# Performance work log

Measured on AMD Instinct MI355X. Metric: run time of the kernel, lower is better.

Reference implementation:

```python
import jax, jax.numpy as jnp
import numpy as np

N_NODES = 50000
N_EDGES = 400000
N_E2E = 1600000
F_N = 128
F_E = 64
H = 128
NEG_SLOPE = 0.2


def setup_inputs() -> dict:
    key = jax.random.key(0)
    ks = jax.random.split(key, 8)
    x_node = jax.random.normal(ks[0], (N_NODES, F_N), dtype=jnp.float32)
    edge_attr = jax.random.normal(ks[1], (N_EDGES, F_E), dtype=jnp.float32)
    edge_index = jax.random.randint(ks[2], (2, N_EDGES), 0, N_NODES, dtype=jnp.int64)
    edge_edge_index = jax.random.randint(ks[3], (2, N_E2E), 0, N_EDGES, dtype=jnp.int64)
    # xavier-uniform-like init scales
    def xavier(k, shape):
        fan_in, fan_out = shape[1], shape[0]
        lim = jnp.sqrt(6.0 / (fan_in + fan_out)).astype(jnp.float32)
        return jax.random.uniform(k, shape, jnp.float32, -lim, lim)
    Wn = xavier(ks[4], (H, F_N))          # lin_node.weight
    We = xavier(ks[5], (H, F_E))          # lin_edge.weight
    an = xavier(ks[6], (1, 2 * H))[0]     # att_n.weight, flattened to [2H]
    ae = xavier(ks[7], (1, 2 * H))[0]     # att_e.weight, flattened to [2H]
    return {"x_node": x_node, "edge_attr": edge_attr, "edge_index": edge_index,
            "edge_edge_index": edge_edge_index, "Wn": Wn, "We": We, "an": an, "ae": ae}


def _segment_softmax(score, seg, num_segments):
    m = jax.ops.segment_max(score, seg, num_segments=num_segments)
    ex = jnp.exp(score - m[seg])
    denom = jax.ops.segment_sum(ex, seg, num_segments=num_segments)
    return ex / denom[seg]


def reference(x_node, edge_attr, edge_index, edge_edge_index, Wn, We, an, ae):
    E = edge_attr.shape[0]
    h = x_node @ Wn.T      # [N, H]
    g = edge_attr @ We.T   # [E, H]

    # ---- node-based neighbors of each edge (its 2 endpoints) ----
    u, v = edge_index[0], edge_index[1]
    e_rep = jnp.concatenate([jnp.arange(E), jnp.arange(E)])   # segment ids [2E]
    n_for_e = jnp.concatenate([u, v])                          # [2E]
    a1, a2 = an[:H], an[H:]   # split cat([g, h]) @ an into two dots
    h_nbr = h[n_for_e]                                         # [2E, H]
    score_ne = jax.nn.leaky_relu(g[e_rep] @ a1 + h_nbr @ a2, NEG_SLOPE)
    alpha_ne = _segment_softmax(score_ne, e_rep, E)
    s_n = jax.ops.segment_sum(alpha_ne[:, None] * h_nbr, e_rep, num_segments=E)
    cnt_n = jax.ops.segment_sum(jnp.ones_like(alpha_ne), e_rep, num_segments=E)
    e_from_nodes = jax.nn.relu(s_n / jnp.maximum(cnt_n, 1.0)[:, None])

    # ---- edge-based neighbors (edges sharing a node) ----
    e_src, e_nbr = edge_edge_index[0], edge_edge_index[1]
    b1, b2 = ae[:H], ae[H:]
    g_nbr = g[e_nbr]                                           # [E2E, H]
    score_ee = jax.nn.leaky_relu(g[e_src] @ b1 + g_nbr @ b2, NEG_SLOPE)
    alpha_ee = _segment_softmax(score_ee, e_src, E)
    s_e = jax.ops.segment_sum(alpha_ee[:, None] * g_nbr, e_src, num_segments=E)
    cnt_e = jax.ops.segment_sum(jnp.ones_like(alpha_ee), e_src, num_segments=E)
    e_from_edges = jax.nn.relu(s_e / jnp.maximum(cnt_e, 1.0)[:, None])

    return jnp.concatenate([e_from_nodes, e_from_edges], axis=-1)  # [E, 2H]
```

## Files before the change

kernel.cpp:

```cpp
#include <hip/hip_runtime.h>
#include <hip/hip_bf16.h>

#define N_NODES 50000
#define N_EDGES 400000
#define N_E2E   1600000
#define F_N 128
#define F_E 64
#define H   128
#define NEG_SLOPE 0.2f
#define CAP 24

typedef __hip_bfloat16 bf16;
typedef __attribute__((ext_vector_type(8))) short bf16x8;
typedef __attribute__((ext_vector_type(4))) float f32x4;


__device__ inline float2 upk(unsigned int v) {
    union { unsigned int u; float f; } a, b;
    a.u = v << 16;
    b.u = v & 0xffff0000u;
    return make_float2(a.f, b.f);
}
__device__ inline unsigned int f2bfbits(float f) {
    union { float f; unsigned int u; } a; a.f = f;
    return (a.u + 0x7fffu + ((a.u >> 16) & 1u)) >> 16;
}
__device__ inline float lrelu(float x) { return x > 0.f ? x : NEG_SLOPE * x; }

__device__ inline float ldf(const void* p, size_t i, int isf32) {
    return isf32 ? ((const float*)p)[i] : __bfloat162float(((const bf16*)p)[i]);
}
__device__ inline int ldidx(const int* p, long long k, int is64) {
    return is64 ? p[2 * k] : p[k];
}

__device__ inline void loadA4(const void* p, int isf32, size_t idx, float* v) {
    if (isf32) {
        const float4 f = *(const float4*)((const float*)p + idx);
        v[0] = f.x; v[1] = f.y; v[2] = f.z; v[3] = f.w;
    } else {
        const uint2 u = *(const uint2*)((const bf16*)p + idx);
        float2 a = upk(u.x), b = upk(u.y);
        v[0] = a.x; v[1] = a.y; v[2] = b.x; v[3] = b.y;
    }
}
__device__ inline void stash(unsigned short* s, unsigned off, unsigned loOff, const float* v) {
    unsigned hb[4], lb[4];
    #pragma unroll
    for (int j = 0; j < 4; ++j) {
        unsigned hbits = f2bfbits(v[j]);
        union { unsigned u; float f; } hf; hf.u = hbits << 16;
        hb[j] = hbits;
        lb[j] = f2bfbits(v[j] - hf.f);
    }
    *(uint2*)((char*)s + off)         = make_uint2(hb[0] | (hb[1] << 16), hb[2] | (hb[3] << 16));
    *(uint2*)((char*)s + loOff + off) = make_uint2(lb[0] | (lb[1] << 16), lb[2] | (lb[3] << 16));
}

__global__ __launch_bounds__(256) void k_pat(unsigned int* __restrict__ o,
                                             long long n, unsigned int pat) {
    long long i = (long long)blockIdx.x * 256 + threadIdx.x;
    long long stride = (long long)gridDim.x * 256;
    for (; i < n; i += stride) o[i] = pat;
}

__global__ __launch_bounds__(256) void k_init(const unsigned int* x, const unsigned int* ea,
                                              const unsigned int* Wn, const unsigned int* We,
                                              const unsigned int* an, const unsigned int* ae,
                                              const unsigned int* ei, const unsigned int* eei,
                                              int* __restrict__ flags, int* __restrict__ cnt) {
    int i = blockIdx.x * 256 + threadIdx.x;
    if (i < N_EDGES) cnt[i] = 0;
    if (blockIdx.x == 0) {
        int t = threadIdx.x;
        if (t < 6) {
            const unsigned int* p = t == 0 ? x : t == 1 ? ea : t == 2 ? Wn
                                  : t == 3 ? We : t == 4 ? an : ae;
            int inrange = 0;
            for (int k = 0; k < 64; k++) {
                unsigned int e = (p[k] >> 7) & 0xFFu;
                if (e >= 100u && e <= 140u) inrange++;
            }
            flags[t] = (inrange < 48) ? 1 : 0;
        } else if (t < 8) {
            const unsigned int* p = (t == 6) ? ei : eei;
            int allzero = 1;
            for (int k = 1; k < 128; k += 2) if (p[k] != 0u) allzero = 0;
            flags[t] = allzero;
        }
    }
}

__global__ __launch_bounds__(256) void k_planes(const void* __restrict__ Wn,
                                                const void* __restrict__ We,
                                                const int* __restrict__ flags,
                                                unsigned short* __restrict__ wnhi,
                                                unsigned short* __restrict__ wnlo,
                                                unsigned short* __restrict__ wehi,
                                                unsigned short* __restrict__ welo) {
    int i = blockIdx.x * 256 + threadIdx.x;
    if (i < 128 * 64) {
        float v = ldf(We, i, flags[3]);
        unsigned hb = f2bfbits(v);
        union { unsigned u; float f; } hf; hf.u = hb << 16;
        wehi[i] = (unsigned short)hb;
        welo[i] = (unsigned short)f2bfbits(v - hf.f);
    } else if (i < 128 * 64 + 128 * 128) {
        int j = i - 128 * 64;
        float v = ldf(Wn, j, flags[2]);
        unsigned hb = f2bfbits(v);
        union { unsigned u; float f; } hf; hf.u = hb << 16;
        wnhi[j] = (unsigned short)hb;
        wnlo[j] = (unsigned short)f2bfbits(v - hf.f);
    }
}

template<int K>
__global__ __launch_bounds__(256) void k_gemm(const void* __restrict__ A,
                                              const int* __restrict__ flags,
                                              int faIdx, int M,
                                              const unsigned short* __restrict__ whi,
                                              const unsigned short* __restrict__ wlo,
                                              bf16* __restrict__ out,
                                              const void* __restrict__ an,
                                              const void* __restrict__ ae,
                                              float* __restrict__ dot0,
                                              float* __restrict__ dot1,
                                              float* __restrict__ dot2) {
    __shared__ unsigned short sA[2 * 128 * 64];
    constexpr unsigned ALO = 128u * 64u * 2u;
    const int t = threadIdx.x;
    const int e0 = blockIdx.x * 128;
    const int fa = flags[faIdx];
    const int w = t >> 6, l = t & 63;
    const int lr = l & 15, lk = l >> 4;
    const unsigned sxor = (unsigned)((l & 7) << 4);

    f32x4 acc[8][2];
    #pragma unroll
    for (int mt = 0; mt < 8; ++mt)
        #pragma unroll
        for (int nt = 0; nt < 2; ++nt)
            acc[mt][nt] = (f32x4){0.f, 0.f, 0.f, 0.f};

    #pragma unroll
    for (int kt = 0; kt < K / 64; ++kt) {
        if (kt) __syncthreads();
        #pragma unroll
        for (int c0 = 0; c0 < 2048; c0 += 256) {
            int c = c0 + t;
            int r = c >> 4, kc = (c & 15) << 2;
            float v[4];
            int e = e0 + r;
            if (e < M) loadA4(A, fa, (size_t)e * K + kt * 64 + kc, v);
            else { v[0] = v[1] = v[2] = v[3] = 0.f; }
            stash(sA, (unsigned)((r * 64 + kc) * 2) ^ ((unsigned)(r & 7) << 4), ALO, v);
        }
        __syncthreads();
        const char* pA = (const char*)sA;
        #pragma unroll
        for (int ks = 0; ks < 2; ++ks) {
            const unsigned ko = (unsigned)((ks * 32 + lk * 8) * 2);
            bf16x8 bh[2], bl[2];
            #pragma unroll
            for (int nt = 0; nt < 2; ++nt) {
                size_t boff = (size_t)(w * 32 + nt * 16 + lr) * K + kt * 64 + ks * 32 + lk * 8;
                bh[nt] = *(const bf16x8*)(whi + boff);
                bl[nt] = *(const bf16x8*)(wlo + boff);
            }
            #pragma unroll
            for (int mt = 0; mt < 8; ++mt) {
                unsigned off = ((unsigned)((mt * 16 + lr) * 128) + ko) ^ sxor;
                bf16x8 ah = *(const bf16x8*)(pA + off);
                bf16x8 al = *(const bf16x8*)(pA + ALO + off);
                #pragma unroll
                for (int nt = 0; nt < 2; ++nt) {
                    acc[mt][nt] = __builtin_amdgcn_mfma_f32_16x16x32_bf16(ah, bh[nt], acc[mt][nt], 0, 0, 0);
                    acc[mt][nt] = __builtin_amdgcn_mfma_f32_16x16x32_bf16(ah, bl[nt], acc[mt][nt], 0, 0, 0);
                    acc[mt][nt] = __builtin_amdgcn_mfma_f32_16x16x32_bf16(al, bh[nt], acc[mt][nt], 0, 0, 0);
                }
            }
        }
    }
    #pragma unroll
    for (int mt = 0; mt < 8; ++mt)
        #pragma unroll
        for (int i = 0; i < 4; ++i) {
            int e = e0 + mt * 16 + lk * 4 + i;
            if (e < M) {
                #pragma unroll
                for (int nt = 0; nt < 2; ++nt)
                    out[(size_t)e * 128 + (w * 32 + nt * 16 + lr)] =
                        __float2bfloat16(acc[mt][nt][i]);
            }
        }
    __syncthreads();
    float* sd = (float*)sA;
    const int fan = flags[4], fae = flags[5];
    const int c0i = w * 32 + lr, c1i = c0i + 16;
    constexpr int ND = (K == 64) ? 3 : 1;
    float av[ND][2];
    if constexpr (K == 64) {
        av[0][0] = ldf(an, c0i, fan);      av[0][1] = ldf(an, c1i, fan);
        av[1][0] = ldf(ae, c0i, fae);      av[1][1] = ldf(ae, c1i, fae);
        av[2][0] = ldf(ae, H + c0i, fae);  av[2][1] = ldf(ae, H + c1i, fae);
    } else {
        av[0][0] = ldf(an, H + c0i, fan);  av[0][1] = ldf(an, H + c1i, fan);
    }
    #pragma unroll
    for (int d = 0; d < ND; ++d)
        #pragma unroll
        for (int mt = 0; mt < 8; ++mt)
            #pragma unroll
            for (int i = 0; i < 4; ++i) {
                float p = acc[mt][0][i] * av[d][0] + acc[mt][1][i] * av[d][1];
                #pragma unroll
                for (int off = 1; off < 16; off <<= 1) p += __shfl_xor(p, off, 64);
                if (lr == 0) sd[(d * 4 + w) * 128 + mt * 16 + lk * 4 + i] = p;
            }
    __syncthreads();
    for (int idx = t; idx < 128 * ND; idx += 256) {
        int d = idx >> 7, row = idx & 127;
        float vs = sd[(d * 4 + 0) * 128 + row] + sd[(d * 4 + 1) * 128 + row]
                 + sd[(d * 4 + 2) * 128 + row] + sd[(d * 4 + 3) * 128 + row];
        int e = e0 + row;
        if (e < M) (d == 0 ? dot0 : d == 1 ? dot1 : dot2)[e] = vs;
    }
}

__global__ __launch_bounds__(256) void k_fill(const int* __restrict__ eei,
                                              const int* __restrict__ flags,
                                              int* __restrict__ cnt,
                                              int* __restrict__ bucket) {
    int k2 = blockIdx.x * 256 + threadIdx.x;
    if (k2 * 2 >= N_E2E) return;
    int is64 = flags[7];
    int s0, s1, n0, n1;
    if (is64) {
        uint4 qs = ((const uint4*)eei)[k2];
        uint4 qn = ((const uint4*)(eei + 2 * (size_t)N_E2E))[k2];
        s0 = (int)qs.x; s1 = (int)qs.z;
        n0 = (int)qn.x; n1 = (int)qn.z;
    } else {
        uint2 qs = ((const uint2*)eei)[k2];
        uint2 qn = ((const uint2*)(eei + (size_t)N_E2E))[k2];
        s0 = (int)qs.x; s1 = (int)qs.y;
        n0 = (int)qn.x; n1 = (int)qn.y;
    }
    int j0 = atomicAdd(&cnt[s0], 1); if (j0 < CAP) bucket[(size_t)s0 * CAP + j0] = n0;
    int j1 = atomicAdd(&cnt[s1], 1); if (j1 < CAP) bucket[(size_t)s1 * CAP + j1] = n1;
}

__global__ __launch_bounds__(256) void k_att(const int* __restrict__ ei,
                                             const int* __restrict__ flags,
                                             const bf16* __restrict__ h,
                                             const float* __restrict__ ha2,
                                             const float* __restrict__ ga1,
                                             const int* __restrict__ cnt,
                                             const int* __restrict__ bucket,
                                             const float* __restrict__ gb1,
                                             const float* __restrict__ gb2,
                                             const bf16* __restrict__ g,
                                             void* __restrict__ out) {
    int e = blockIdx.x * 8 + (threadIdx.x >> 5);
    int lane = threadIdx.x & 31;
    int base = threadIdx.x & 32;
    int is64 = flags[6], fo = flags[0];

    int c = cnt[e]; if (c > CAP) c = CAP;
    int u = ldidx(ei, e, is64);
    int v = ldidx(ei, (long long)N_EDGES + e, is64);
    float s = -1e30f; int mynbr = 0;
    if (lane < c) {
        mynbr = bucket[(size_t)e * CAP + lane];
        s = lrelu(gb1[e] + gb2[mynbr]);
    }

    float ga = ga1[e];
    float su = lrelu(ga + ha2[u]);
    float sv = lrelu(ga + ha2[v]);
    float mn = fmaxf(su, sv);
    float eu = __expf(su - mn), ev = __expf(sv - mn);
    float inv = 1.f / (eu + ev);
    float wu = (eu * inv) * 0.5f;
    float wv = (ev * inv) * 0.5f;
    const uint2* hw = (const uint2*)h;
    uint2 qu = hw[(size_t)u * 32 + lane];
    uint2 qv = hw[(size_t)v * 32 + lane];
    float2 u0 = upk(qu.x), u1 = upk(qu.y);
    float2 v0 = upk(qv.x), v1 = upk(qv.y);
    float c0 = wu * u0.x + wv * v0.x;
    float c1 = wu * u0.y + wv * v0.y;
    float c2 = wu * u1.x + wv * v1.x;
    float c3 = wu * u1.y + wv * v1.y;
    float nr0 = c0 > 0.f ? c0 : 0.f; if (c0 != c0) nr0 = c0;
    float nr1 = c1 > 0.f ? c1 : 0.f; if (c1 != c1) nr1 = c1;
    float nr2 = c2 > 0.f ? c2 : 0.f; if (c2 != c2) nr2 = c2;
    float nr3 = c3 > 0.f ? c3 : 0.f; if (c3 != c3) nr3 = c3;

    float m = s;
    #pragma unroll
    for (int off = 16; off; off >>= 1) m = fmaxf(m, __shfl_xor(m, off, 64));
    float ex = (lane < c) ? __expf(s - m) : 0.f;
    float denom = ex;
    #pragma unroll
    for (int off = 16; off; off >>= 1) denom += __shfl_xor(denom, off, 64);
    float invd = denom > 0.f ? 1.f / denom : 0.f;
    float ax = 0.f, ay = 0.f, az = 0.f, aw = 0.f;
    const uint2* __restrict__ gw = (const uint2*)g;
    for (int j0 = 0; j0 < c; j0 += 4) {
        float a0 = __shfl(ex, base + j0, 64) * invd;
        float a1 = __shfl(ex, base + j0 + 1, 64) * invd;
        float a2 = __shfl(ex, base + j0 + 2, 64) * invd;
        float a3 = __shfl(ex, base + j0 + 3, 64) * invd;
        int n0 = __shfl(mynbr, base + j0, 64);
        int n1 = __shfl(mynbr, base + j0 + 1, 64);
        int n2 = __shfl(mynbr, base + j0 + 2, 64);
        int n3 = __shfl(mynbr, base + j0 + 3, 64);
        uint2 q0 = gw[(size_t)n0 * 32 + lane];
        uint2 q1 = gw[(size_t)n1 * 32 + lane];
        uint2 q2 = gw[(size_t)n2 * 32 + lane];
        uint2 q3 = gw[(size_t)n3 * 32 + lane];
        float2 l0 = upk(q0.x), h0 = upk(q0.y);
        float2 l1 = upk(q1.x), h1 = upk(q1.y);
        float2 l2 = upk(q2.x), h2 = upk(q2.y);
        float2 l3 = upk(q3.x), h3 = upk(q3.y);
        ax += a0 * l0.x; ay += a0 * l0.y; az += a0 * h0.x; aw += a0 * h0.y;
        ax += a1 * l1.x; ay += a1 * l1.y; az += a1 * h1.x; aw += a1 * h1.y;
        ax += a2 * l2.x; ay += a2 * l2.y; az += a2 * h2.x; aw += a2 * h2.y;
        ax += a3 * l3.x; ay += a3 * l3.y; az += a3 * h3.x; aw += a3 * h3.y;
    }
    float invc = 1.f / (float)(c > 0 ? c : 1);
    ax *= invc; ay *= invc; az *= invc; aw *= invc;
    float er0 = ax > 0.f ? ax : 0.f; if (ax != ax) er0 = ax;
    float er1 = ay > 0.f ? ay : 0.f; if (ay != ay) er1 = ay;
    float er2 = az > 0.f ? az : 0.f; if (az != az) er2 = az;
    float er3 = aw > 0.f ? aw : 0.f; if (aw != aw) er3 = aw;

    if (fo) {
        float4* o0 = (float4*)((float*)out + (size_t)e * 256 + 4 * lane);
        *o0 = make_float4(nr0, nr1, nr2, nr3);
        float4* o1 = (float4*)((float*)out + (size_t)e * 256 + H + 4 * lane);
        *o1 = make_float4(er0, er1, er2, er3);
    } else {
        uint2 pk0, pk1;
        pk0.x = f2bfbits(nr0) | (f2bfbits(nr1) << 16);
        pk0.y = f2bfbits(nr2) | (f2bfbits(nr3) << 16);
        pk1.x = f2bfbits(er0) | (f2bfbits(er1) << 16);
        pk1.y = f2bfbits(er2) | (f2bfbits(er3) << 16);
        ((uint2*)((bf16*)out + (size_t)e * 256))[lane] = pk0;
        ((uint2*)((bf16*)out + (size_t)e * 256 + H))[lane] = pk1;
    }
}

extern "C" void kernel_launch(void* const* d_in, const int* in_sizes, int n_in,
                              void* d_out, int out_size, void* d_ws, size_t ws_size,
                              hipStream_t stream) {
    (void)out_size;
    unsigned int* outw = (unsigned int*)d_out;
    const long long OUTW = (long long)N_EDGES * 256 / 2;

    const int* s = in_sizes;
    auto isEI  = [](int v) { return v == 2 * N_EDGES || v == 4 * N_EDGES; };
    auto isEEI = [](int v) { return v == 2 * N_E2E || v == 4 * N_E2E; };
    bool okA = n_in == 8 && s[0] == N_NODES * F_N && s[1] == N_EDGES * F_E &&
               isEI(s[2]) && isEEI(s[3]) && s[4] == H * F_N && s[5] == H * F_E &&
               s[6] == 2 * H && s[7] == 2 * H;
    bool okB = n_in == 8 && s[0] == H * F_E && s[1] == H * F_N && s[2] == 2 * H &&
               s[3] == 2 * H && s[4] == N_EDGES * F_E && isEEI(s[5]) && isEI(s[6]) &&
               s[7] == N_NODES * F_N;
    if (!okA && !okB) {
        k_pat<<<2048, 256, 0, stream>>>(outw, OUTW, 0x44804480u);
        return;
    }
    const void *x, *ea, *Wn, *We, *an, *ae; const int *ei, *eei;
    if (okA) {
        x = d_in[0]; ea = d_in[1]; ei = (const int*)d_in[2]; eei = (const int*)d_in[3];
        Wn = d_in[4]; We = d_in[5]; an = d_in[6]; ae = d_in[7];
    } else {
        We = d_in[0]; Wn = d_in[1]; ae = d_in[2]; an = d_in[3];
        ea = d_in[4]; eei = (const int*)d_in[5]; ei = (const int*)d_in[6]; x = d_in[7];
    }

    char* w0 = (char*)d_ws; char* w = w0;
    auto alloc = [&](size_t bytes) -> char* {
        char* p = w; w += (bytes + 255) & ~(size_t)255; return p;
    };
    int*   flags  = (int*)alloc(256);
    float* ha2    = (float*)alloc((size_t)N_NODES * 4);
    float* ga1    = (float*)alloc((size_t)N_EDGES * 4);
    float* gb1    = (float*)alloc((size_t)N_EDGES * 4);
    float* gb2    = (float*)alloc((size_t)N_EDGES * 4);
    int*   cnt    = (int*)alloc((size_t)N_EDGES * 4);
    int*   bucket = (int*)alloc((size_t)N_EDGES * CAP * 4);
    bf16*  h      = (bf16*)alloc((size_t)N_NODES * H * 2);
    bf16*  g      = (bf16*)alloc((size_t)N_EDGES * H * 2);
    unsigned short* wnhi = (unsigned short*)alloc(128 * 128 * 2);
    unsigned short* wnlo = (unsigned short*)alloc(128 * 128 * 2);
    unsigned short* wehi = (unsigned short*)alloc(128 * 64 * 2);
    unsigned short* welo = (unsigned short*)alloc(128 * 64 * 2);
    if ((size_t)(w - w0) > ws_size) {
        k_pat<<<2048, 256, 0, stream>>>(outw, OUTW, 0x44004400u);
        return;
    }


    k_init<<<(N_EDGES + 255) / 256, 256, 0, stream>>>((const unsigned int*)x,
            (const unsigned int*)ea, (const unsigned int*)Wn, (const unsigned int*)We,
            (const unsigned int*)an, (const unsigned int*)ae,
            (const unsigned int*)ei, (const unsigned int*)eei, flags, cnt);
    k_planes<<<96, 256, 0, stream>>>(Wn, We, flags, wnhi, wnlo, wehi, welo);
    k_gemm<128><<<(N_NODES + 127) / 128, 256, 0, stream>>>(x, flags, 0, N_NODES,
            wnhi, wnlo, h, an, ae, ha2, nullptr, nullptr);
    k_gemm<64><<<N_EDGES / 128, 256, 0, stream>>>(ea, flags, 1, N_EDGES,
            wehi, welo, g, an, ae, ga1, gb1, gb2);
    k_fill<<<(N_E2E / 2 + 255) / 256, 256, 0, stream>>>(eei, flags, cnt, bucket);
    k_att<<<N_EDGES / 8, 256, 0, stream>>>(ei, flags, h, ha2, ga1,
                                           cnt, bucket, gb1, gb2, g, d_out);
}
```

Baseline: 938.1 us.

## Pack neighbor score into bucket entries and reorder launches, smaller node GEMM tile

The fill kernel now gathers gb2 for each neighbor and stores it next to the neighbor index in a uint2 bucket. The attention kernel then reads the score term in the same load instead of doing a dependent random gather. To allow this, the edge GEMM and fill now run before the node GEMM. The node GEMM is templated on row tile size and uses 64-row tiles, which gives it more blocks. The cost is a bucket that is twice as large, plus random gb2 reads that move into the fill kernel.

New measurement: 913.7 us. 2.6% less time.

```diff
diff --git a/kernel.cpp b/kernel.cpp
--- a/kernel.cpp
+++ b/kernel.cpp
@@ -115,7 +115,7 @@
     }
 }
 
-template<int K>
+template<int K, int TM>
 __global__ __launch_bounds__(256) void k_gemm(const void* __restrict__ A,
                                               const int* __restrict__ flags,
                                               int faIdx, int M,
@@ -127,18 +127,19 @@
                                               float* __restrict__ dot0,
                                               float* __restrict__ dot1,
                                               float* __restrict__ dot2) {
-    __shared__ unsigned short sA[2 * 128 * 64];
-    constexpr unsigned ALO = 128u * 64u * 2u;
+    constexpr int MT = TM / 16;
+    __shared__ unsigned short sA[2 * TM * 64];
+    constexpr unsigned ALO = (unsigned)TM * 64u * 2u;
     const int t = threadIdx.x;
-    const int e0 = blockIdx.x * 128;
+    const int e0 = blockIdx.x * TM;
     const int fa = flags[faIdx];
     const int w = t >> 6, l = t & 63;
     const int lr = l & 15, lk = l >> 4;
     const unsigned sxor = (unsigned)((l & 7) << 4);
 
-    f32x4 acc[8][2];
-    #pragma unroll
-    for (int mt = 0; mt < 8; ++mt)
+    f32x4 acc[MT][2];
+    #pragma unroll
+    for (int mt = 0; mt < MT; ++mt)
         #pragma unroll
         for (int nt = 0; nt < 2; ++nt)
             acc[mt][nt] = (f32x4){0.f, 0.f, 0.f, 0.f};
@@ -147,7 +148,7 @@
     for (int kt = 0; kt < K / 64; ++kt) {
         if (kt) __syncthreads();
         #pragma unroll
-        for (int c0 = 0; c0 < 2048; c0 += 256) {
+        for (int c0 = 0; c0 < TM * 16; c0 += 256) {
             int c = c0 + t;
             int r = c >> 4, kc = (c & 15) << 2;
             float v[4];
@@ -169,7 +170,7 @@
                 bl[nt] = *(const bf16x8*)(wlo + boff);
             }
             #pragma unroll
-            for (int mt = 0; mt < 8; ++mt) {
+            for (int mt = 0; mt < MT; ++mt) {
                 unsigned off = ((unsigned)((mt * 16 + lr) * 128) + ko) ^ sxor;
                 bf16x8 ah = *(const bf16x8*)(pA + off);
                 bf16x8 al = *(const bf16x8*)(pA + ALO + off);
@@ -183,7 +184,7 @@
         }
     }
     #pragma unroll
-    for (int mt = 0; mt < 8; ++mt)
+    for (int mt = 0; mt < MT; ++mt)
         #pragma unroll
         for (int i = 0; i < 4; ++i) {
             int e = e0 + mt * 16 + lk * 4 + i;
@@ -210,19 +211,19 @@
     #pragma unroll
     for (int d = 0; d < ND; ++d)
         #pragma unroll
-        for (int mt = 0; mt < 8; ++mt)
+        for (int mt = 0; mt < MT; ++mt)
             #pragma unroll
             for (int i = 0; i < 4; ++i) {
                 float p = acc[mt][0][i] * av[d][0] + acc[mt][1][i] * av[d][1];
                 #pragma unroll
                 for (int off = 1; off < 16; off <<= 1) p += __shfl_xor(p, off, 64);
-                if (lr == 0) sd[(d * 4 + w) * 128 + mt * 16 + lk * 4 + i] = p;
+                if (lr == 0) sd[(d * 4 + w) * TM + mt * 16 + lk * 4 + i] = p;
             }
     __syncthreads();
-    for (int idx = t; idx < 128 * ND; idx += 256) {
-        int d = idx >> 7, row = idx & 127;
-        float vs = sd[(d * 4 + 0) * 128 + row] + sd[(d * 4 + 1) * 128 + row]
-                 + sd[(d * 4 + 2) * 128 + row] + sd[(d * 4 + 3) * 128 + row];
+    for (int idx = t; idx < TM * ND; idx += 256) {
+        int d = idx / TM, row = idx % TM;
+        float vs = sd[(d * 4 + 0) * TM + row] + sd[(d * 4 + 1) * TM + row]
+                 + sd[(d * 4 + 2) * TM + row] + sd[(d * 4 + 3) * TM + row];
         int e = e0 + row;
         if (e < M) (d == 0 ? dot0 : d == 1 ? dot1 : dot2)[e] = vs;
     }
@@ -230,8 +231,9 @@
 
 __global__ __launch_bounds__(256) void k_fill(const int* __restrict__ eei,
                                               const int* __restrict__ flags,
+                                              const float* __restrict__ gb2,
                                               int* __restrict__ cnt,
-                                              int* __restrict__ bucket) {
+                                              uint2* __restrict__ bucket) {
     int k2 = blockIdx.x * 256 + threadIdx.x;
     if (k2 * 2 >= N_E2E) return;
     int is64 = flags[7];
@@ -247,8 +249,13 @@
         s0 = (int)qs.x; s1 = (int)qs.y;
         n0 = (int)qn.x; n1 = (int)qn.y;
     }
-    int j0 = atomicAdd(&cnt[s0], 1); if (j0 < CAP) bucket[(size_t)s0 * CAP + j0] = n0;
-    int j1 = atomicAdd(&cnt[s1], 1); if (j1 < CAP) bucket[(size_t)s1 * CAP + j1] = n1;
+    union { float f; unsigned u; } g0, g1;
+    g0.f = gb2[n0];
+    g1.f = gb2[n1];
+    int j0 = atomicAdd(&cnt[s0], 1);
+    if (j0 < CAP) bucket[(size_t)s0 * CAP + j0] = make_uint2((unsigned)n0, g0.u);
+    int j1 = atomicAdd(&cnt[s1], 1);
+    if (j1 < CAP) bucket[(size_t)s1 * CAP + j1] = make_uint2((unsigned)n1, g1.u);
 }
 
 __global__ __launch_bounds__(256) void k_att(const int* __restrict__ ei,
@@ -257,9 +264,8 @@
                                              const float* __restrict__ ha2,
                                              const float* __restrict__ ga1,
                                              const int* __restrict__ cnt,
-                                             const int* __restrict__ bucket,
+                                             const uint2* __restrict__ bucket,
                                              const float* __restrict__ gb1,
-                                             const float* __restrict__ gb2,
                                              const bf16* __restrict__ g,
                                              void* __restrict__ out) {
     int e = blockIdx.x * 8 + (threadIdx.x >> 5);
@@ -272,8 +278,10 @@
     int v = ldidx(ei, (long long)N_EDGES + e, is64);
     float s = -1e30f; int mynbr = 0;
     if (lane < c) {
-        mynbr = bucket[(size_t)e * CAP + lane];
-        s = lrelu(gb1[e] + gb2[mynbr]);
+        uint2 q = bucket[(size_t)e * CAP + lane];
+        mynbr = (int)q.x;
+        union { unsigned u; float f; } gq; gq.u = q.y;
+        s = lrelu(gb1[e] + gq.f);
     }
 
     float ga = ga1[e];
@@ -392,7 +400,7 @@
     float* gb1    = (float*)alloc((size_t)N_EDGES * 4);
     float* gb2    = (float*)alloc((size_t)N_EDGES * 4);
     int*   cnt    = (int*)alloc((size_t)N_EDGES * 4);
-    int*   bucket = (int*)alloc((size_t)N_EDGES * CAP * 4);
+    uint2* bucket = (uint2*)alloc((size_t)N_EDGES * CAP * 8);
     bf16*  h      = (bf16*)alloc((size_t)N_NODES * H * 2);
     bf16*  g      = (bf16*)alloc((size_t)N_EDGES * H * 2);
     unsigned short* wnhi = (unsigned short*)alloc(128 * 128 * 2);
@@ -410,11 +418,11 @@
             (const unsigned int*)an, (const unsigned int*)ae,
             (const unsigned int*)ei, (const unsigned int*)eei, flags, cnt);
     k_planes<<<96, 256, 0, stream>>>(Wn, We, flags, wnhi, wnlo, wehi, welo);
-    k_gemm<128><<<(N_NODES + 127) / 128, 256, 0, stream>>>(x, flags, 0, N_NODES,
+    k_gemm<64, 128><<<N_EDGES / 128, 256, 0, stream>>>(ea, flags, 1, N_EDGES,
+            wehi, welo, g, an, ae, ga1, gb1, gb2);
+    k_fill<<<(N_E2E / 2 + 255) / 256, 256, 0, stream>>>(eei, flags, gb2, cnt, bucket);
+    k_gemm<128, 64><<<(N_NODES + 63) / 64, 256, 0, stream>>>(x, flags, 0, N_NODES,
             wnhi, wnlo, h, an, ae, ha2, nullptr, nullptr);
-    k_gemm<64><<<N_EDGES / 128, 256, 0, stream>>>(ea, flags, 1, N_EDGES,
-            wehi, welo, g, an, ae, ga1, gb1, gb2);
-    k_fill<<<(N_E2E / 2 + 255) / 256, 256, 0, stream>>>(eei, flags, cnt, bucket);
     k_att<<<N_EDGES / 8, 256, 0, stream>>>(ei, flags, h, ha2, ga1,
-                                           cnt, bucket, gb1, gb2, g, d_out);
-}
+                                           cnt, bucket, gb1, g, d_out);
+}
```
